# Kernel tuning notes

Hardware: AMD Instinct MI355X
Metric: run time of the kernel (lower is better)

Reference implementation:

```python
import jax, jax.numpy as jnp
import numpy as np

D_MODEL = 512
D_AUX = 64
B, E = 8, 2048


def setup_inputs() -> dict:
    key = jax.random.key(0)
    ks = jax.random.split(key, 12)
    x = jax.random.normal(ks[0], (B, E, D_MODEL), dtype=jnp.float32)
    query_aux = jax.random.normal(ks[1], (B, E, D_AUX), dtype=jnp.float32)
    key_aux = jax.random.normal(ks[2], (B, E, D_AUX), dtype=jnp.float32)
    adjacency_mask = jax.random.randint(ks[3], (B, E, E), 0, 2, dtype=jnp.int32)
    merge_coefficients = jax.random.uniform(ks[4], (B, E, E), dtype=jnp.float32)
    # learned parameters of IrregularityAwareAttention (nn.Linear weights stored
    # as (out, in) in torch; we keep (in, out) for x @ W)
    s = 1.0 / np.sqrt(D_MODEL)
    Wq = jax.random.uniform(ks[5], (D_MODEL, D_MODEL), minval=-s, maxval=s, dtype=jnp.float32)
    bq = jax.random.uniform(ks[6], (D_MODEL,), minval=-s, maxval=s, dtype=jnp.float32)
    Wk = jax.random.uniform(ks[7], (D_MODEL, D_MODEL), minval=-s, maxval=s, dtype=jnp.float32)
    bk = jax.random.uniform(ks[8], (D_MODEL,), minval=-s, maxval=s, dtype=jnp.float32)
    Wv = jax.random.uniform(ks[9], (D_MODEL, D_MODEL), minval=-s, maxval=s, dtype=jnp.float32)
    bv = jax.random.uniform(ks[10], (D_MODEL,), minval=-s, maxval=s, dtype=jnp.float32)
    threshold = jnp.float32(0.5)
    return {
        "x": x, "query_aux": query_aux, "key_aux": key_aux,
        "adjacency_mask": adjacency_mask, "merge_coefficients": merge_coefficients,
        "Wq": Wq, "bq": bq, "Wk": Wk, "bk": bk, "Wv": Wv, "bv": bv,
        "threshold": threshold,
    }


def reference(x, query_aux, key_aux, adjacency_mask, merge_coefficients,
              Wq, bq, Wk, bk, Wv, bv, threshold):
    d_model = x.shape[-1]
    scale = jnp.asarray(d_model, x.dtype) ** 0.5
    q = x @ Wq + bq                      # (B, E, D)
    k = x @ Wk + bk
    v = x @ Wv + bv
    scores = jnp.einsum("bed,bfd->bef", q, k) / scale   # (B, E, E)

    aux_scale = jnp.asarray(key_aux.shape[-1], x.dtype) ** 0.5
    scores_aux = jnp.einsum("bed,bfd->bef", query_aux, key_aux) / aux_scale

    non_zero_mask = scores_aux != 0
    positive_mask = scores > threshold
    merge_mask = positive_mask & non_zero_mask
    blended = (1.0 - merge_coefficients) * scores + merge_coefficients * scores_aux
    scores = jnp.where(merge_mask, blended, scores)

    mask_value = jnp.finfo(scores.dtype).min
    scores = jnp.where(adjacency_mask == 0, mask_value, scores)

    attn = jax.nn.softmax(scores, axis=-1)
    return jnp.einsum("bef,bfd->bed", attn, v)
```

## Files before the change

kernel.cpp:

```cpp
#include <hip/hip_runtime.h>

#define E2 2048
#define DM 512

typedef __attribute__((ext_vector_type(8))) _Float16 half8;
typedef __attribute__((ext_vector_type(4))) _Float16 half4;
typedef __attribute__((ext_vector_type(8))) short short8;
typedef __attribute__((ext_vector_type(4))) short shortx4;
typedef __attribute__((ext_vector_type(4))) float floatx4;

__device__ __forceinline__ void stage_tile(const _Float16* __restrict__ g, int stride,
                                           _Float16* lds, int tid) {
  const int r0 = tid >> 2;
  const int c0 = (tid & 3) * 8;
  const int wbase = (tid >> 6) * 512;
#pragma unroll
  for (int h = 0; h < 2; ++h) {
    const _Float16* gp = g + (size_t)(h * 64 + r0) * stride + c0;
    _Float16* lp = lds + h * 2048 + wbase;
    __builtin_amdgcn_global_load_lds(
        (const __attribute__((address_space(1))) unsigned int*)gp,
        (__attribute__((address_space(3))) unsigned int*)lp, 16, 0, 0);
  }
}

__device__ __forceinline__ void stage_tile8(const _Float16* __restrict__ g, int stride,
                                            _Float16* lds, int tid) {
  const int r0 = tid >> 2;
  const int c0 = (tid & 3) * 8;
  const int wbase = (tid >> 6) * 512;
  const _Float16* gp = g + (size_t)r0 * stride + c0;
  __builtin_amdgcn_global_load_lds(
      (const __attribute__((address_space(1))) unsigned int*)gp,
      (__attribute__((address_space(3))) unsigned int*)(lds + wbase), 16, 0, 0);
}

__device__ __forceinline__ void mfma16(const _Float16* As, const _Float16* Bs,
                                       floatx4 acc[4][4], int wm, int wn, int lane) {
  const int m16 = lane & 15, quad = lane >> 4;
  half8 a[4];
#pragma unroll
  for (int i = 0; i < 4; ++i)
    a[i] = *(const half8*)(As + (wm * 64 + i * 16 + m16) * 32 + quad * 8);
#pragma unroll
  for (int j = 0; j < 4; ++j) {
    const half8 b = *(const half8*)(Bs + (wn * 64 + j * 16 + m16) * 32 + quad * 8);
#pragma unroll
    for (int i = 0; i < 4; ++i)
      acc[i][j] = __builtin_amdgcn_mfma_f32_16x16x32_f16(a[i], b, acc[i][j], 0, 0, 0);
  }
}

__device__ __forceinline__ void mfma8(const _Float16* As, const _Float16* Bs,
                                      floatx4 acc[4][2], int wm, int wn, int lane) {
  const int m16 = lane & 15, quad = lane >> 4;
  half8 a[4];
#pragma unroll
  for (int i = 0; i < 4; ++i)
    a[i] = *(const half8*)(As + (wm * 64 + i * 16 + m16) * 32 + quad * 8);
#pragma unroll
  for (int j = 0; j < 2; ++j) {
    const half8 b = *(const half8*)(Bs + (wn * 32 + j * 16 + m16) * 32 + quad * 8);
#pragma unroll
    for (int i = 0; i < 4; ++i)
      acc[i][j] = __builtin_amdgcn_mfma_f32_16x16x32_f16(a[i], b, acc[i][j], 0, 0, 0);
  }
}

__device__ __forceinline__ void mfma24(const _Float16* Ah, const _Float16* Al,
                                       const _Float16* Bh, const _Float16* Bl,
                                       floatx4 acc[4][2], int wm, int wn, int lane) {
  const int m16 = lane & 15, quad = lane >> 4;
  half8 ah[4], al[4];
#pragma unroll
  for (int i = 0; i < 4; ++i) {
    const int off = (wm * 64 + i * 16 + m16) * 32 + quad * 8;
    ah[i] = *(const half8*)(Ah + off);
    al[i] = *(const half8*)(Al + off);
  }
#pragma unroll
  for (int j = 0; j < 2; ++j) {
    const int off = (wn * 32 + j * 16 + m16) * 32 + quad * 8;
    const half8 bh = *(const half8*)(Bh + off);
    const half8 bl = *(const half8*)(Bl + off);
#pragma unroll
    for (int i = 0; i < 4; ++i) {
      acc[i][j] = __builtin_amdgcn_mfma_f32_16x16x32_f16(ah[i], bh, acc[i][j], 0, 0, 0);
      acc[i][j] = __builtin_amdgcn_mfma_f32_16x16x32_f16(al[i], bh, acc[i][j], 0, 0, 0);
      acc[i][j] = __builtin_amdgcn_mfma_f32_16x16x32_f16(ah[i], bl, acc[i][j], 0, 0, 0);
    }
  }
}

__global__ void split_conv_k(const float* __restrict__ src, _Float16* __restrict__ hi,
                             _Float16* __restrict__ lo, float scale, int n8) {
  int i = blockIdx.x * blockDim.x + threadIdx.x;
  const int stride = gridDim.x * blockDim.x;
  const float4* s4 = (const float4*)src;
  for (; i < n8; i += stride) {
    const float4 u = s4[2 * i], v = s4[2 * i + 1];
    const float g[8] = {u.x, u.y, u.z, u.w, v.x, v.y, v.z, v.w};
    half8 h, l;
#pragma unroll
    for (int t = 0; t < 8; ++t) {
      const float gv = g[t] * scale;
      const _Float16 hv = (_Float16)gv;
      h[t] = hv;
      l[t] = (_Float16)(gv - (float)hv);
    }
    ((half8*)hi)[i] = h;
    ((half8*)lo)[i] = l;
  }
}

__global__ void conv_k(const float* __restrict__ src, _Float16* __restrict__ dst, int n8) {
  int i = blockIdx.x * blockDim.x + threadIdx.x;
  const int stride = gridDim.x * blockDim.x;
  const float4* s4 = (const float4*)src;
  for (; i < n8; i += stride) {
    const float4 u = s4[2 * i], v = s4[2 * i + 1];
    const float g[8] = {u.x, u.y, u.z, u.w, v.x, v.y, v.z, v.w};
    half8 h;
#pragma unroll
    for (int t = 0; t < 8; ++t) h[t] = (_Float16)g[t];
    ((half8*)dst)[i] = h;
  }
}

__global__ void transw_k(const float* __restrict__ Wq, const float* __restrict__ Wk,
                         const float* __restrict__ Wv, _Float16* __restrict__ Wth,
                         _Float16* __restrict__ Wtl) {
  const int z = blockIdx.z;
  const float* W = (z == 0) ? Wq : (z == 1) ? Wk : Wv;
  __shared__ float t[32][33];
  const int n0 = blockIdx.x * 32, k0 = blockIdx.y * 32;
  const int tx = threadIdx.x, ty = threadIdx.y;
#pragma unroll
  for (int i = 0; i < 32; i += 8) t[ty + i][tx] = W[(size_t)(k0 + ty + i) * DM + n0 + tx];
  __syncthreads();
  const size_t zb = (size_t)z * DM * DM;
#pragma unroll
  for (int i = 0; i < 32; i += 8) {
    const float g = t[tx][ty + i] * 64.0f;
    const _Float16 h = (_Float16)g;
    const size_t o = zb + (size_t)(n0 + ty + i) * DM + (k0 + tx);
    Wth[o] = h;
    Wtl[o] = (_Float16)(g - (float)h);
  }
}

__global__ __launch_bounds__(512, 4) void qkv_k(
    const _Float16* __restrict__ xh, const _Float16* __restrict__ xl,
    const _Float16* __restrict__ Wth, const _Float16* __restrict__ Wtl,
    const float* __restrict__ bqp, const float* __restrict__ bkp,
    const float* __restrict__ bvp,
    _Float16* __restrict__ qh, _Float16* __restrict__ ql,
    _Float16* __restrict__ kh, _Float16* __restrict__ kl,
    _Float16* __restrict__ vT) {
  __shared__ _Float16 Ah[2][4096], Al[2][4096], Bh[2][4096], Bl[2][4096];
  const int tid = threadIdx.x, lane = tid & 63, wv = tid >> 6;
  const int wm = wv >> 2, wn = wv & 3;
  const int bm = blockIdx.x, bn = blockIdx.y, z = blockIdx.z;
  const bool split = (z < 2);
  const _Float16* Ash = xh + (size_t)bm * 128 * DM;
  const _Float16* Asl = xl + (size_t)bm * 128 * DM;
  const _Float16* Bsh = Wth + ((size_t)z * DM + bn * 128) * DM;
  const _Float16* Bsl = Wtl + ((size_t)z * DM + bn * 128) * DM;
  floatx4 acc[4][2];
  const floatx4 z4 = {0.f, 0.f, 0.f, 0.f};
#pragma unroll
  for (int i = 0; i < 4; ++i)
#pragma unroll
    for (int j = 0; j < 2; ++j) acc[i][j] = z4;

  stage_tile8(Ash, DM, Ah[0], tid);
  stage_tile8(Bsh, DM, Bh[0], tid);
  if (split) { stage_tile8(Asl, DM, Al[0], tid); stage_tile8(Bsl, DM, Bl[0], tid); }
  __syncthreads();
  for (int kt = 0; kt < 16; ++kt) {
    const int cur = kt & 1, nxt = cur ^ 1;
    if (kt < 15) {
      const int ko = (kt + 1) * 32;
      stage_tile8(Ash + ko, DM, Ah[nxt], tid);
      stage_tile8(Bsh + ko, DM, Bh[nxt], tid);
      if (split) { stage_tile8(Asl + ko, DM, Al[nxt], tid); stage_tile8(Bsl + ko, DM, Bl[nxt], tid); }
    }
    if (split) mfma24(Ah[cur], Al[cur], Bh[cur], Bl[cur], acc, wm, wn, lane);
    else       mfma8(Ah[cur], Bh[cur], acc, wm, wn, lane);
    __syncthreads();
  }
  const int m16 = lane & 15, quad = lane >> 4;
  const float* bias = (z == 0) ? bqp : (z == 1) ? bkp : bvp;
  if (split) {
    _Float16* oh = (z == 0) ? qh : kh;
    _Float16* ol = (z == 0) ? ql : kl;
#pragma unroll
    for (int j = 0; j < 2; ++j) {
      const int n = bn * 128 + wn * 32 + j * 16 + m16;
      const float bb = bias[n];
#pragma unroll
      for (int i = 0; i < 4; ++i) {
        const int m = bm * 128 + wm * 64 + i * 16 + quad * 4;
#pragma unroll
        for (int r = 0; r < 4; ++r) {
          const float val = acc[i][j][r] * (1.0f / 256.0f) + bb;
          const float v8 = val * 8.0f;
          const _Float16 h = (_Float16)v8;
          const _Float16 l = (_Float16)(v8 - (float)h);
          const size_t o = (size_t)(m + r) * DM + n;
          oh[o] = h; ol[o] = l;
        }
      }
    }
  } else {
#pragma unroll
    for (int j = 0; j < 2; ++j) {
      const int n = bn * 128 + wn * 32 + j * 16 + m16;
      const float bb = bias[n];
#pragma unroll
      for (int i = 0; i < 4; ++i) {
        const int m = bm * 128 + wm * 64 + i * 16 + quad * 4;
        const int bidx = m >> 11, e0 = m & 2047;
        half4 pk;
#pragma unroll
        for (int r = 0; r < 4; ++r)
          pk[r] = (_Float16)(acc[i][j][r] * (1.0f / 256.0f) + bb);
        *(half4*)(vT + ((size_t)bidx * DM + n) * E2 + e0) = pk;
      }
    }
  }
}

__global__ __launch_bounds__(512, 4) void scores_k(
    const _Float16* __restrict__ qh, const _Float16* __restrict__ ql,
    const _Float16* __restrict__ kh, const _Float16* __restrict__ kl,
    const _Float16* __restrict__ qah, const _Float16* __restrict__ kah,
    const int* __restrict__ adj, const float* __restrict__ mc,
    const float* __restrict__ thrp, unsigned short* __restrict__ sc) {
  __shared__ _Float16 S[32768];
  _Float16* const AhB = S;
  _Float16* const AlB = S + 8192;
  _Float16* const BhB = S + 16384;
  _Float16* const BlB = S + 24576;
  const int tid = threadIdx.x, lane = tid & 63, wv = tid >> 6;
  const int wm = wv >> 2, wn = wv & 3;
  const int bf = blockIdx.x, be = blockIdx.y, b = blockIdx.z;
  const _Float16* Ash = qh + ((size_t)b * E2 + be * 128) * DM;
  const _Float16* Asl = ql + ((size_t)b * E2 + be * 128) * DM;
  const _Float16* Bsh = kh + ((size_t)b * E2 + bf * 128) * DM;
  const _Float16* Bsl = kl + ((size_t)b * E2 + bf * 128) * DM;
  floatx4 accm[4][2];
  const floatx4 z4 = {0.f, 0.f, 0.f, 0.f};
#pragma unroll
  for (int i = 0; i < 4; ++i)
#pragma unroll
    for (int j = 0; j < 2; ++j) accm[i][j] = z4;

  stage_tile8(Ash, DM, AhB, tid);
  stage_tile8(Bsh, DM, BhB, tid);
  stage_tile8(Asl, DM, AlB, tid);
  stage_tile8(Bsl, DM, BlB, tid);
  __syncthreads();
  for (int kt = 0; kt < 16; ++kt) {
    const int cur = kt & 1, nxt = cur ^ 1;
    if (kt < 15) {
      const int ko = (kt + 1) * 32;
      stage_tile8(Ash + ko, DM, AhB + nxt * 4096, tid);
      stage_tile8(Bsh + ko, DM, BhB + nxt * 4096, tid);
      stage_tile8(Asl + ko, DM, AlB + nxt * 4096, tid);
      stage_tile8(Bsl + ko, DM, BlB + nxt * 4096, tid);
    }
    mfma24(AhB + cur * 4096, AlB + cur * 4096, BhB + cur * 4096, BlB + cur * 4096,
           accm, wm, wn, lane);
    __syncthreads();
  }
  floatx4 acca[4][2];
#pragma unroll
  for (int i = 0; i < 4; ++i)
#pragma unroll
    for (int j = 0; j < 2; ++j) acca[i][j] = z4;
  const _Float16* A2 = qah + ((size_t)b * E2 + be * 128) * 64;
  const _Float16* B2 = kah + ((size_t)b * E2 + bf * 128) * 64;
  stage_tile8(A2, 64, AhB, tid);
  stage_tile8(B2, 64, BhB, tid);
  stage_tile8(A2 + 32, 64, AhB + 4096, tid);
  stage_tile8(B2 + 32, 64, BhB + 4096, tid);
  __syncthreads();
  mfma8(AhB, BhB, acca, wm, wn, lane);
  mfma8(AhB + 4096, BhB + 4096, acca, wm, wn, lane);

  float* const sL = (float*)S;
  _Float16* const saL = S + 16896;
  const float thr = *thrp;
  const int m16 = lane & 15, quad = lane >> 4;
#pragma unroll
  for (int h = 0; h < 2; ++h) {
    __syncthreads();
    if (wm == h) {
#pragma unroll
      for (int j = 0; j < 2; ++j) {
        const int cl = wn * 32 + j * 16 + m16;
#pragma unroll
        for (int i = 0; i < 4; ++i) {
#pragma unroll
          for (int r = 0; r < 4; ++r) {
            const int rl = i * 16 + quad * 4 + r;
            sL[rl * 132 + cl] = accm[i][j][r] * (0.015625f * 0.044194173824159216f);
            saL[rl * 132 + cl] = (_Float16)(acca[i][j][r] * 0.125f);
          }
        }
      }
    }
    __syncthreads();
    const size_t rowbase = (size_t)b * E2 + be * 128 + h * 64;
#pragma unroll
    for (int g = 0; g < 4; ++g) {
      const int tf = g * 2048 + tid * 4;
      const int rl = tf >> 7, cl = tf & 127;
      const size_t idx = (rowbase + rl) * E2 + bf * 128 + cl;
      const int4 a4 = *(const int4*)(adj + idx);
      const float4 c4 = *(const float4*)(mc + idx);
      const float4 s4v = *(const float4*)(sL + rl * 132 + cl);
      const half4 sa4 = *(const half4*)(saL + rl * 132 + cl);
      const float ss[4] = {s4v.x, s4v.y, s4v.z, s4v.w};
      const int aa[4] = {a4.x, a4.y, a4.z, a4.w};
      const float cc[4] = {c4.x, c4.y, c4.z, c4.w};
      shortx4 o;
#pragma unroll
      for (int t = 0; t < 4; ++t) {
        float s = ss[t];
        const float sa = (float)sa4[t];
        if (sa != 0.0f && s > thr) s = (1.0f - cc[t]) * s + cc[t] * sa;
        unsigned short ov;
        if (aa[t] == 0) {
          ov = 0xFBFFu;
        } else {
          union { _Float16 hh; unsigned short u; } u;
          u.hh = (_Float16)s;
          ov = u.u;
        }
        o[t] = (short)ov;
      }
      *(shortx4*)(sc + idx) = o;
    }
  }
}

__global__ __launch_bounds__(256) void softmax_k(unsigned short* __restrict__ sc) {
  const size_t row = blockIdx.x;
  unsigned short* p = sc + row * E2;
  const int tid = threadIdx.x, lane = tid & 63, wv = tid >> 6;
  const short8 raw = *(const short8*)(p + tid * 8);
  float f[8];
#pragma unroll
  for (int t = 0; t < 8; ++t) {
    union { _Float16 h; short s; } u; u.s = raw[t];
    f[t] = (float)u.h;
  }
  float mx = f[0];
#pragma unroll
  for (int t = 1; t < 8; ++t) mx = fmaxf(mx, f[t]);
#pragma unroll
  for (int o = 32; o > 0; o >>= 1) mx = fmaxf(mx, __shfl_xor(mx, o, 64));
  __shared__ float red[8];
  if (lane == 0) red[wv] = mx;
  __syncthreads();
  mx = fmaxf(fmaxf(red[0], red[1]), fmaxf(red[2], red[3]));
  float ef[8], sum = 0.f;
#pragma unroll
  for (int t = 0; t < 8; ++t) { ef[t] = __expf(f[t] - mx); sum += ef[t]; }
#pragma unroll
  for (int o = 32; o > 0; o >>= 1) sum += __shfl_xor(sum, o, 64);
  if (lane == 0) red[4 + wv] = sum;
  __syncthreads();
  sum = (red[4] + red[5]) + (red[6] + red[7]);
  const float inv = 1.0f / sum;
  short8 ov;
#pragma unroll
  for (int t = 0; t < 8; ++t) {
    union { _Float16 h; short s; } u;
    u.h = (_Float16)(ef[t] * inv);
    ov[t] = u.s;
  }
  *(short8*)(p + tid * 8) = ov;
}

__global__ __launch_bounds__(256, 2) void pv_k(
    const _Float16* __restrict__ at, const _Float16* __restrict__ vT,
    float* __restrict__ out) {
  __shared__ _Float16 As[2][4096], Bs[2][4096];
  const int tid = threadIdx.x, lane = tid & 63, wv = tid >> 6;
  const int wm = wv >> 1, wn = wv & 1;
  const int bd = blockIdx.x, be = blockIdx.y, b = blockIdx.z;
  const _Float16* Asrc = at + ((size_t)b * E2 + be * 128) * E2;
  const _Float16* Bsrc = vT + ((size_t)b * DM + bd * 128) * E2;
  floatx4 acc[4][4];
  const floatx4 z4 = {0.f, 0.f, 0.f, 0.f};
#pragma unroll
  for (int i = 0; i < 4; ++i)
#pragma unroll
    for (int j = 0; j < 4; ++j) acc[i][j] = z4;
  stage_tile(Asrc, E2, As[0], tid);
  stage_tile(Bsrc, E2, Bs[0], tid);
  __syncthreads();
  for (int kt = 0; kt < 64; ++kt) {
    const int cur = kt & 1, nxt = cur ^ 1;
    if (kt < 63) {
      const int ko = (kt + 1) * 32;
      stage_tile(Asrc + ko, E2, As[nxt], tid);
      stage_tile(Bsrc + ko, E2, Bs[nxt], tid);
    }
    mfma16(As[cur], Bs[cur], acc, wm, wn, lane);
    __syncthreads();
  }
  const int m16 = lane & 15, quad = lane >> 4;
#pragma unroll
  for (int j = 0; j < 4; ++j) {
    const int d = bd * 128 + wn * 64 + j * 16 + m16;
#pragma unroll
    for (int i = 0; i < 4; ++i) {
      const int e0 = be * 128 + wm * 64 + i * 16 + quad * 4;
#pragma unroll
      for (int r = 0; r < 4; ++r)
        out[((size_t)b * E2 + e0 + r) * DM + d] = acc[i][j][r];
    }
  }
}

extern "C" void kernel_launch(void* const* d_in, const int* in_sizes, int n_in,
                              void* d_out, int out_size, void* d_ws, size_t ws_size,
                              hipStream_t stream) {
  const float* x   = (const float*)d_in[0];
  const float* qa  = (const float*)d_in[1];
  const float* ka  = (const float*)d_in[2];
  const int*   adj = (const int*)d_in[3];
  const float* mc  = (const float*)d_in[4];
  const float* Wq  = (const float*)d_in[5];
  const float* bq  = (const float*)d_in[6];
  const float* Wk  = (const float*)d_in[7];
  const float* bk  = (const float*)d_in[8];
  const float* Wv  = (const float*)d_in[9];
  const float* bv  = (const float*)d_in[10];
  const float* thr = (const float*)d_in[11];
  float* out = (float*)d_out;
  char* w = (char*)d_ws;
  const size_t MiB = 1ull << 20;
  _Float16* xh  = (_Float16*)(w + 0 * MiB);
  _Float16* xl  = (_Float16*)(w + 16 * MiB);
  _Float16* qhp = (_Float16*)(w + 32 * MiB);
  _Float16* qlp = (_Float16*)(w + 48 * MiB);
  _Float16* khp = (_Float16*)(w + 64 * MiB);
  _Float16* klp = (_Float16*)(w + 80 * MiB);
  _Float16* vT  = (_Float16*)(w + 96 * MiB);
  _Float16* Wth = (_Float16*)(w + 112 * MiB);
  _Float16* Wtl = (_Float16*)(w + 114 * MiB);
  _Float16* qah = (_Float16*)(w + 116 * MiB);
  _Float16* kah = (_Float16*)(w + 118 * MiB);
  unsigned short* sc = (unsigned short*)(w + 120 * MiB);

  split_conv_k<<<2048, 256, 0, stream>>>(x, xh, xl, 4.0f, (8 * E2 * DM) / 8);
  conv_k<<<256, 256, 0, stream>>>(qa, qah, (8 * E2 * 64) / 8);
  conv_k<<<256, 256, 0, stream>>>(ka, kah, (8 * E2 * 64) / 8);
  transw_k<<<dim3(16, 16, 3), dim3(32, 8), 0, stream>>>(Wq, Wk, Wv, Wth, Wtl);
  qkv_k<<<dim3(128, 4, 3), 512, 0, stream>>>(xh, xl, Wth, Wtl, bq, bk, bv,
                                             qhp, qlp, khp, klp, vT);
  scores_k<<<dim3(16, 16, 8), 512, 0, stream>>>(qhp, qlp, khp, klp, qah, kah,
                                                adj, mc, thr, sc);
  softmax_k<<<16384, 256, 0, stream>>>(sc);
  pv_k<<<dim3(4, 16, 8), 256, 0, stream>>>((const _Float16*)sc, vT, out);
}
```

Before: 580.0 us.

## Prefetch adjacency/merge tiles during QK GEMM and raise wave priority around MFMA

```diff
diff --git a/kernel.cpp b/kernel.cpp
--- a/kernel.cpp
+++ b/kernel.cpp
@@ -185,8 +185,10 @@
       stage_tile8(Bsh + ko, DM, Bh[nxt], tid);
       if (split) { stage_tile8(Asl + ko, DM, Al[nxt], tid); stage_tile8(Bsl + ko, DM, Bl[nxt], tid); }
     }
+    __builtin_amdgcn_s_setprio(1);
     if (split) mfma24(Ah[cur], Al[cur], Bh[cur], Bl[cur], acc, wm, wn, lane);
     else       mfma8(Ah[cur], Bh[cur], acc, wm, wn, lane);
+    __builtin_amdgcn_s_setprio(0);
     __syncthreads();
   }
   const int m16 = lane & 15, quad = lane >> 4;
@@ -256,11 +258,16 @@
 #pragma unroll
     for (int j = 0; j < 2; ++j) accm[i][j] = z4;
 
+  const size_t rowbase0 = (size_t)b * E2 + be * 128;
+  int4 pa0[4];
+  float4 pc0[4];
+
   stage_tile8(Ash, DM, AhB, tid);
   stage_tile8(Bsh, DM, BhB, tid);
   stage_tile8(Asl, DM, AlB, tid);
   stage_tile8(Bsl, DM, BlB, tid);
   __syncthreads();
+#pragma unroll
   for (int kt = 0; kt < 16; ++kt) {
     const int cur = kt & 1, nxt = cur ^ 1;
     if (kt < 15) {
@@ -270,8 +277,18 @@
       stage_tile8(Asl + ko, DM, AlB + nxt * 4096, tid);
       stage_tile8(Bsl + ko, DM, BlB + nxt * 4096, tid);
     }
+    if (kt == 1 || kt == 4 || kt == 7 || kt == 10) {
+      const int g = (kt - 1) / 3;
+      const int tf = g * 2048 + tid * 4;
+      const int rl = tf >> 7, cl = tf & 127;
+      const size_t idx = (rowbase0 + rl) * E2 + bf * 128 + cl;
+      pa0[g] = *(const int4*)(adj + idx);
+      pc0[g] = *(const float4*)(mc + idx);
+    }
+    __builtin_amdgcn_s_setprio(1);
     mfma24(AhB + cur * 4096, AlB + cur * 4096, BhB + cur * 4096, BlB + cur * 4096,
            accm, wm, wn, lane);
+    __builtin_amdgcn_s_setprio(0);
     __syncthreads();
   }
   floatx4 acca[4][2];
@@ -286,63 +303,114 @@
   stage_tile8(A2 + 32, 64, AhB + 4096, tid);
   stage_tile8(B2 + 32, 64, BhB + 4096, tid);
   __syncthreads();
+  __builtin_amdgcn_s_setprio(1);
   mfma8(AhB, BhB, acca, wm, wn, lane);
   mfma8(AhB + 4096, BhB + 4096, acca, wm, wn, lane);
+  __builtin_amdgcn_s_setprio(0);
 
   float* const sL = (float*)S;
   _Float16* const saL = S + 16896;
   const float thr = *thrp;
   const int m16 = lane & 15, quad = lane >> 4;
-#pragma unroll
-  for (int h = 0; h < 2; ++h) {
-    __syncthreads();
-    if (wm == h) {
-#pragma unroll
-      for (int j = 0; j < 2; ++j) {
-        const int cl = wn * 32 + j * 16 + m16;
-#pragma unroll
-        for (int i = 0; i < 4; ++i) {
-#pragma unroll
-          for (int r = 0; r < 4; ++r) {
-            const int rl = i * 16 + quad * 4 + r;
-            sL[rl * 132 + cl] = accm[i][j][r] * (0.015625f * 0.044194173824159216f);
-            saL[rl * 132 + cl] = (_Float16)(acca[i][j][r] * 0.125f);
-          }
+  int4 pa1[4]; float4 pc1[4];
+
+  __syncthreads();
+  if (wm == 0) {
+#pragma unroll
+    for (int j = 0; j < 2; ++j) {
+      const int cl = wn * 32 + j * 16 + m16;
+#pragma unroll
+      for (int i = 0; i < 4; ++i) {
+#pragma unroll
+        for (int r = 0; r < 4; ++r) {
+          const int rl = i * 16 + quad * 4 + r;
+          sL[rl * 132 + cl] = accm[i][j][r] * (0.015625f * 0.044194173824159216f);
+          saL[rl * 132 + cl] = (_Float16)(acca[i][j][r] * 0.125f);
         }
       }
     }
-    __syncthreads();
-    const size_t rowbase = (size_t)b * E2 + be * 128 + h * 64;
-#pragma unroll
-    for (int g = 0; g < 4; ++g) {
-      const int tf = g * 2048 + tid * 4;
-      const int rl = tf >> 7, cl = tf & 127;
-      const size_t idx = (rowbase + rl) * E2 + bf * 128 + cl;
-      const int4 a4 = *(const int4*)(adj + idx);
-      const float4 c4 = *(const float4*)(mc + idx);
-      const float4 s4v = *(const float4*)(sL + rl * 132 + cl);
-      const half4 sa4 = *(const half4*)(saL + rl * 132 + cl);
-      const float ss[4] = {s4v.x, s4v.y, s4v.z, s4v.w};
-      const int aa[4] = {a4.x, a4.y, a4.z, a4.w};
-      const float cc[4] = {c4.x, c4.y, c4.z, c4.w};
-      shortx4 o;
-#pragma unroll
-      for (int t = 0; t < 4; ++t) {
-        float s = ss[t];
-        const float sa = (float)sa4[t];
-        if (sa != 0.0f && s > thr) s = (1.0f - cc[t]) * s + cc[t] * sa;
-        unsigned short ov;
-        if (aa[t] == 0) {
-          ov = 0xFBFFu;
-        } else {
-          union { _Float16 hh; unsigned short u; } u;
-          u.hh = (_Float16)s;
-          ov = u.u;
+  }
+  __syncthreads();
+#pragma unroll
+  for (int g = 0; g < 4; ++g) {
+    const int tf = g * 2048 + tid * 4;
+    const int rl = tf >> 7, cl = tf & 127;
+    const size_t idx = (rowbase0 + rl) * E2 + bf * 128 + cl;
+    const int4 a4 = pa0[g];
+    const float4 c4 = pc0[g];
+    const float4 s4v = *(const float4*)(sL + rl * 132 + cl);
+    const half4 sa4 = *(const half4*)(saL + rl * 132 + cl);
+    const size_t idx1 = idx + (size_t)64 * E2;
+    pa1[g] = *(const int4*)(adj + idx1);
+    pc1[g] = *(const float4*)(mc + idx1);
+    const float ss[4] = {s4v.x, s4v.y, s4v.z, s4v.w};
+    const int aa[4] = {a4.x, a4.y, a4.z, a4.w};
+    const float cc[4] = {c4.x, c4.y, c4.z, c4.w};
+    shortx4 o;
+#pragma unroll
+    for (int t = 0; t < 4; ++t) {
+      float s = ss[t];
+      const float sa = (float)sa4[t];
+      if (sa != 0.0f && s > thr) s = (1.0f - cc[t]) * s + cc[t] * sa;
+      unsigned short ov;
+      if (aa[t] == 0) {
+        ov = 0xFBFFu;
+      } else {
+        union { _Float16 hh; unsigned short u; } u;
+        u.hh = (_Float16)s;
+        ov = u.u;
+      }
+      o[t] = (short)ov;
+    }
+    *(shortx4*)(sc + idx) = o;
+  }
+
+  __syncthreads();
+  if (wm == 1) {
+#pragma unroll
+    for (int j = 0; j < 2; ++j) {
+      const int cl = wn * 32 + j * 16 + m16;
+#pragma unroll
+      for (int i = 0; i < 4; ++i) {
+#pragma unroll
+        for (int r = 0; r < 4; ++r) {
+          const int rl = i * 16 + quad * 4 + r;
+          sL[rl * 132 + cl] = accm[i][j][r] * (0.015625f * 0.044194173824159216f);
+          saL[rl * 132 + cl] = (_Float16)(acca[i][j][r] * 0.125f);
         }
-        o[t] = (short)ov;
       }
-      *(shortx4*)(sc + idx) = o;
-    }
+    }
+  }
+  __syncthreads();
+#pragma unroll
+  for (int g = 0; g < 4; ++g) {
+    const int tf = g * 2048 + tid * 4;
+    const int rl = tf >> 7, cl = tf & 127;
+    const size_t idx = (rowbase0 + 64 + rl) * E2 + bf * 128 + cl;
+    const int4 a4 = pa1[g];
+    const float4 c4 = pc1[g];
+    const float4 s4v = *(const float4*)(sL + rl * 132 + cl);
+    const half4 sa4 = *(const half4*)(saL + rl * 132 + cl);
+    const float ss[4] = {s4v.x, s4v.y, s4v.z, s4v.w};
+    const int aa[4] = {a4.x, a4.y, a4.z, a4.w};
+    const float cc[4] = {c4.x, c4.y, c4.z, c4.w};
+    shortx4 o;
+#pragma unroll
+    for (int t = 0; t < 4; ++t) {
+      float s = ss[t];
+      const float sa = (float)sa4[t];
+      if (sa != 0.0f && s > thr) s = (1.0f - cc[t]) * s + cc[t] * sa;
+      unsigned short ov;
+      if (aa[t] == 0) {
+        ov = 0xFBFFu;
+      } else {
+        union { _Float16 hh; unsigned short u; } u;
+        u.hh = (_Float16)s;
+        ov = u.u;
+      }
+      o[t] = (short)ov;
+    }
+    *(shortx4*)(sc + idx) = o;
   }
 }
 
@@ -410,7 +478,9 @@
       stage_tile(Asrc + ko, E2, As[nxt], tid);
       stage_tile(Bsrc + ko, E2, Bs[nxt], tid);
     }
+    __builtin_amdgcn_s_setprio(1);
     mfma16(As[cur], Bs[cur], acc, wm, wn, lane);
+    __builtin_amdgcn_s_setprio(0);
     __syncthreads();
   }
   const int m16 = lane & 15, quad = lane >> 4;
```

Result: slower. 642.4 us (+10.8%).
